# Performance work log

Hardware: AMD Instinct MI355X
Metric: run time of the kernel (lower is better)

The kernel has to match this reference:

```python
import jax, jax.numpy as jnp
import numpy as np

B, T, H, HW = 16, 32, 512, 32  # batch, timesteps, hidden channels, spatial size


def setup_inputs() -> dict:
    key = jax.random.key(0)
    k1, k2, k3, k4, k5 = jax.random.split(key, 5)
    x = jax.random.normal(k1, (B, T, HW, HW), dtype=jnp.float32)
    # cell conv: 1x1, (1 + H) -> 4H, with bias (k=1 default, padding 'same')
    W_conv = jax.random.normal(k2, (4 * H, 1 + H, 1, 1), dtype=jnp.float32) * 0.02
    b_conv = jax.random.normal(k3, (4 * H,), dtype=jnp.float32) * 0.02
    # post conv: 3x3, H -> 1, padding 'same'
    W_post = jax.random.normal(k4, (1, H, 3, 3), dtype=jnp.float32) * 0.02
    b_post = jax.random.normal(k5, (1,), dtype=jnp.float32) * 0.02
    return {"x": x, "W_conv": W_conv, "b_conv": b_conv, "W_post": W_post, "b_post": b_post}


def _post_conv(h, W_post, b_post):
    # NCHW 3x3 'same' conv
    y = jax.lax.conv_general_dilated(
        h, W_post, window_strides=(1, 1), padding="SAME",
        dimension_numbers=("NCHW", "OIHW", "NCHW"))
    return y + b_post[None, :, None, None]


def reference(x, W_conv, b_conv, W_post, b_post):
    Wc = W_conv[:, :, 0, 0]  # [4H, 1+H] -- 1x1 conv is a channel GEMM

    def step(carry, xt):
        h, c = carry  # [B,H,32,32] each; xt [B,1,32,32]
        z = jnp.concatenate([xt, h], axis=1)  # [B,1+H,32,32]
        gates = jnp.einsum("bchw,oc->bohw", z, Wc) + b_conv[None, :, None, None]
        i, f, o, g = jnp.split(gates, 4, axis=1)
        # Faithful to source (non-standard gating):
        c = jax.nn.sigmoid(f) * c + jax.nn.sigmoid(i) + jnp.tanh(g)
        h = jax.nn.sigmoid(o) + jnp.tanh(c)
        y = _post_conv(h, W_post, b_post)  # [B,1,32,32]
        return (h, c), y

    h0 = jnp.zeros((x.shape[0], H, HW, HW), dtype=x.dtype)
    c0 = jnp.zeros_like(h0)
    xs = x[:, :, None, :, :].transpose(1, 0, 2, 3, 4)  # [T,B,1,32,32]
    _, ys = jax.lax.scan(step, (h0, c0), xs)  # ys [T,B,1,32,32]
    out = ys[:, :, 0].transpose(1, 0, 2, 3)  # [B,T,32,32] == cat along dim=1
    return out
```

## Files before the change

### kernel.cpp

```cpp
#include <hip/hip_runtime.h>
#include <cstdint>
#include <cstddef>

#define B_    16
#define T_    32
#define H_    512
#define P_    1024
#define NPOS  16384
#define NG    2048

typedef __attribute__((ext_vector_type(8))) short short8;
typedef __attribute__((ext_vector_type(4))) float f32x4;

__device__ __forceinline__ unsigned short f2bf(float f) {
  uint32_t u = __float_as_uint(f);
  u += 0x7fffu + ((u >> 16) & 1u);
  return (unsigned short)(u >> 16);
}
__device__ __forceinline__ float bflo(uint32_t u) { return __uint_as_float(u << 16); }
__device__ __forceinline__ float bfhi(uint32_t u) { return __uint_as_float(u & 0xffff0000u); }

__device__ __forceinline__ float sigf(float x) {
  return __builtin_amdgcn_rcpf(1.0f + __expf(-x));
}
__device__ __forceinline__ float tanhf_(float x) {
  return 1.0f - 2.0f * __builtin_amdgcn_rcpf(__expf(2.0f * x) + 1.0f);
}

__device__ __forceinline__ void gload_lds16(const void* g, void* l) {
  __builtin_amdgcn_global_load_lds(
      (const __attribute__((address_space(1))) void*)g,
      (__attribute__((address_space(3))) void*)l, 16, 0, 0);
}

__global__ void repack_w(const float* __restrict__ Wc, const float* __restrict__ bconv,
                         unsigned short* __restrict__ Wp, float* __restrict__ w0x,
                         float* __restrict__ bx) {
  int idx = blockIdx.x * 256 + threadIdx.x;
  int r = idx >> 9, k = idx & 511;
  int ch = r >> 2, g = r & 3;
  int o = g * 512 + ch;
  Wp[idx] = f2bf(Wc[o * 513 + 1 + k]);
  if (k == 0) { w0x[r] = Wc[o * 513]; bx[r] = bconv[o]; }
}

__global__ void repack_wpost(const float* __restrict__ Wpost, unsigned short* __restrict__ wppb) {
  int idx = blockIdx.x * 256 + threadIdx.x;
  if (idx >= 16 * 512) return;
  int j = idx >> 9, c = idx & 511;
  float v = (j < 9) ? Wpost[c * 9 + j] : 0.f;
  unsigned short hi = f2bf(v);
  float lo = v - bflo((uint32_t)hi);
  wppb[idx] = hi;
  wppb[16 * 512 + idx] = f2bf(lo);
}

__global__ __launch_bounds__(256, 2)
void lstm_step(const unsigned short* __restrict__ Wp,
               const unsigned short* __restrict__ hprev,
               unsigned short* __restrict__ hnext,
               _Float16* __restrict__ Cst,
               const float* __restrict__ w0x, const float* __restrict__ bxv,
               const float* __restrict__ xin,
               const unsigned short* __restrict__ wppb,
               float* __restrict__ up, int t) {
  __shared__ unsigned short As[256 * 64];
  __shared__ unsigned short Bs[128 * 64];

  const int tid = threadIdx.x;
  const int lane = tid & 63;
  const int wv = tid >> 6;
  const int wm = wv >> 1, wn = wv & 1;
  const int q = lane >> 4, l = lane & 15;

  const int lid = blockIdx.x;
  const int xcd = lid & 7;
  const int s   = lid >> 3;
  const int ny  = xcd * 16 + (s & 15);
  const int rx  = s >> 4;
  const int r0  = rx * 256;
  const int n0  = ny * 128;
  const int ch0 = rx * 64;

  const int srow = tid >> 3;
  const int lchunk = (tid & 7) ^ (srow & 7);
  const unsigned short* gA = Wp    + (size_t)(r0 + srow) * 512 + lchunk * 8;
  const unsigned short* gB = hprev + (size_t)(n0 + srow) * 512 + lchunk * 8;
  char* lA = (char*)As + wv * 1024;
  char* lB = (char*)Bs + wv * 1024;

  f32x4 acc[8][4] = {};

  for (int kc = 0; kc < 512; kc += 64) {
#pragma unroll
    for (int j = 0; j < 8; ++j)
      gload_lds16(gA + (size_t)j * (32 * 512) + kc, lA + j * 4096);
#pragma unroll
    for (int j = 0; j < 4; ++j)
      gload_lds16(gB + (size_t)j * (32 * 512) + kc, lB + j * 4096);
    __syncthreads();

#pragma unroll
    for (int kk = 0; kk < 2; ++kk) {
      short8 af[8], bf_[4];
#pragma unroll
      for (int mi = 0; mi < 8; ++mi) {
        int row = wm * 128 + mi * 16 + l;
        int sidx = row * 64 + (((kk * 4 + q) ^ (row & 7)) * 8);
        af[mi] = *(const short8*)(As + sidx);
      }
#pragma unroll
      for (int ni = 0; ni < 4; ++ni) {
        int row = wn * 64 + ni * 16 + l;
        int sidx = row * 64 + (((kk * 4 + q) ^ (row & 7)) * 8);
        bf_[ni] = *(const short8*)(Bs + sidx);
      }
#pragma unroll
      for (int mi = 0; mi < 8; ++mi)
#pragma unroll
        for (int ni = 0; ni < 4; ++ni)
          acc[mi][ni] = __builtin_amdgcn_mfma_f32_16x16x32_bf16(af[mi], bf_[ni], acc[mi][ni], 0, 0, 0);
    }
    __syncthreads();
  }

  float xv[4]; int posL[4]; size_t cbase[4];
#pragma unroll
  for (int ni = 0; ni < 4; ++ni) {
    posL[ni] = wn * 64 + ni * 16 + l;
    int pos = n0 + posL[ni];
    int b = pos >> 10, p = pos & 1023;
    xv[ni] = xin[((b * T_ + t) << 10) + p];
    cbase[ni] = ((size_t)b << 19) + p;
  }
#pragma unroll
  for (int mi = 0; mi < 8; ++mi) {
    int chl = wm * 32 + mi * 4 + q;
    int rg = r0 + wm * 128 + mi * 16 + q * 4;
    float4 w0 = *(const float4*)(w0x + rg);
    float4 bb = *(const float4*)(bxv + rg);
    int ch = ch0 + chl;
#pragma unroll
    for (int ni = 0; ni < 4; ++ni) {
      f32x4 g = acc[mi][ni];
      float gi = g[0] + w0.x * xv[ni] + bb.x;
      float gf = g[1] + w0.y * xv[ni] + bb.y;
      float go = g[2] + w0.z * xv[ni] + bb.z;
      float gg = g[3] + w0.w * xv[ni] + bb.w;
      size_t cidx = cbase[ni] + ((size_t)ch << 10);
      float cold = (float)Cst[cidx];
      float cn = sigf(gf) * cold + sigf(gi) + tanhf_(gg);
      float hn = sigf(go) + tanhf_(cn);
      Cst[cidx] = (_Float16)cn;
      As[posL[ni] * 64 + (chl ^ ((posL[ni] & 7) << 3))] = f2bf(hn);
    }
  }
  __syncthreads();

  {
    int pl = tid >> 1;
    int cb2 = (tid & 1) << 2;
    const unsigned short* srcrow = As + pl * 64;
    unsigned short* dst = hnext + (size_t)(n0 + pl) * 512 + ch0 + (cb2 << 3);
#pragma unroll
    for (int i = 0; i < 4; ++i)
      ((uint4*)dst)[i] = *(const uint4*)(srcrow + (((cb2 + i) ^ (pl & 7)) << 3));
  }

  {
    const unsigned short* wb_hi = wppb;
    const unsigned short* wb_lo = wppb + 16 * 512;
    const int posg = wv * 32;
    f32x4 a2[2] = {};
#pragma unroll
    for (int kk = 0; kk < 2; ++kk) {
      const int wo = l * 512 + ch0 + kk * 32 + q * 8;
      short8 whi = *(const short8*)(wb_hi + wo);
      short8 wlo = *(const short8*)(wb_lo + wo);
#pragma unroll
      for (int ni2 = 0; ni2 < 2; ++ni2) {
        int row = posg + ni2 * 16 + l;
        int sidx = row * 64 + (((kk * 4 + q) ^ (row & 7)) * 8);
        short8 hf = *(const short8*)(As + sidx);
        a2[ni2] = __builtin_amdgcn_mfma_f32_16x16x32_bf16(whi, hf, a2[ni2], 0, 0, 0);
        a2[ni2] = __builtin_amdgcn_mfma_f32_16x16x32_bf16(wlo, hf, a2[ni2], 0, 0, 0);
      }
    }
#pragma unroll
    for (int ni2 = 0; ni2 < 2; ++ni2) {
      int pix = n0 + posg + ni2 * 16 + l;
#pragma unroll
      for (int r = 0; r < 4; ++r) {
        int j = q * 4 + r;
        if (j < 9)
          up[(size_t)(rx * 9 + j) * NPOS + pix] = a2[ni2][r];
      }
    }
  }
}

__global__ __launch_bounds__(256)
void conv_st2(const float* __restrict__ up, const float* __restrict__ bpost,
              float* __restrict__ out, int t) {
  int idx = blockIdx.x * 256 + threadIdx.x;
  int b = idx >> 10, p = idx & 1023;
  int py = p >> 5, px = p & 31;
  float acc = bpost[0];
#pragma unroll
  for (int dy = -1; dy <= 1; ++dy) {
    int ny = py + dy;
    if ((unsigned)ny > 31u) continue;
#pragma unroll
    for (int dx = -1; dx <= 1; ++dx) {
      int nx = px + dx;
      if ((unsigned)nx > 31u) continue;
      int j = (dy + 1) * 3 + (dx + 1);
      int np = (b << 10) + (ny << 5) + nx;
#pragma unroll
      for (int rx = 0; rx < 8; ++rx)
        acc += up[(size_t)(rx * 9 + j) * NPOS + np];
    }
  }
  out[((b * T_ + t) << 10) + p] = acc;
}

extern "C" void kernel_launch(void* const* d_in, const int* in_sizes, int n_in,
                              void* d_out, int out_size, void* d_ws, size_t ws_size,
                              hipStream_t stream) {
  const float* x     = (const float*)d_in[0];
  const float* Wconv = (const float*)d_in[1];
  const float* bconv = (const float*)d_in[2];
  const float* Wpost = (const float*)d_in[3];
  const float* bpost = (const float*)d_in[4];
  float* out = (float*)d_out;
  char* ws = (char*)d_ws;

  unsigned short* h0   = (unsigned short*)(ws);
  unsigned short* h1   = (unsigned short*)(ws + 16777216);
  _Float16*       Cst  = (_Float16*)(ws + 33554432);
  unsigned short* Wp   = (unsigned short*)(ws + 50331648);
  float*          w0x  = (float*)(ws + 52428800);
  float*          bx   = (float*)(ws + 52436992);
  unsigned short* wppb = (unsigned short*)(ws + 52445184);
  float*          up   = (float*)(ws + 52477952);

  hipMemsetAsync(h0, 0, 16777216, stream);
  hipMemsetAsync(Cst, 0, 16777216, stream);
  repack_w<<<4096, 256, 0, stream>>>(Wconv, bconv, Wp, w0x, bx);
  repack_wpost<<<32, 256, 0, stream>>>(Wpost, wppb);

  unsigned short* hp = h0;
  unsigned short* hn = h1;
  for (int t = 0; t < T_; ++t) {
    lstm_step<<<1024, 256, 0, stream>>>(Wp, hp, hn, Cst, w0x, bx, x, wppb, up, t);
    conv_st2<<<64, 256, 0, stream>>>(up, bpost, out, t);
    unsigned short* tmp = hp; hp = hn; hn = tmp;
  }
}
```

Before: 1.763 ms.

## Fold previous step's post-conv reduction into next LSTM step with double-buffered partials

The separate conv_st2 launch after every timestep is removed. Instead, the first 16 threads of each lstm_step block reduce the previous step's 3x3 post-conv partial sums for 16 pixels and write out[t-1], with the partial buffer now double-buffered across steps; a single conv_st2 launch handles the final step. The GEMM's first K-chunk global->LDS loads are issued before this extra work, and each later chunk load is moved to the end of the previous iteration. The intent is to cut 31 small kernel launches and their serialization gaps. The cost is extra scattered reads in a few threads of each GEMM block and one more workspace buffer.

```diff
diff --git a/kernel.cpp b/kernel.cpp
--- a/kernel.cpp
+++ b/kernel.cpp
@@ -63,7 +63,8 @@
                const float* __restrict__ w0x, const float* __restrict__ bxv,
                const float* __restrict__ xin,
                const unsigned short* __restrict__ wppb,
-               float* __restrict__ up, int t) {
+               const float* __restrict__ upPrev, float* __restrict__ upCur,
+               const float* __restrict__ bpost, float* __restrict__ out, int t) {
   __shared__ unsigned short As[256 * 64];
   __shared__ unsigned short Bs[128 * 64];
 
@@ -91,13 +92,37 @@
 
   f32x4 acc[8][4] = {};
 
+#pragma unroll
+  for (int j = 0; j < 8; ++j)
+    gload_lds16(gA + (size_t)j * (32 * 512), lA + j * 4096);
+#pragma unroll
+  for (int j = 0; j < 4; ++j)
+    gload_lds16(gB + (size_t)j * (32 * 512), lB + j * 4096);
+
+  if (t > 0 && tid < 16) {
+    int pix = lid * 16 + tid;
+    int b = pix >> 10, p = pix & 1023;
+    int py = p >> 5, px = p & 31;
+    float a = bpost[0];
+#pragma unroll
+    for (int dy = -1; dy <= 1; ++dy) {
+      int nyy = py + dy;
+      if ((unsigned)nyy > 31u) continue;
+#pragma unroll
+      for (int dx = -1; dx <= 1; ++dx) {
+        int nx = px + dx;
+        if ((unsigned)nx > 31u) continue;
+        int j = (dy + 1) * 3 + (dx + 1);
+        int np = (b << 10) + (nyy << 5) + nx;
+#pragma unroll
+        for (int rr = 0; rr < 8; ++rr)
+          a += upPrev[(size_t)(rr * 9 + j) * NPOS + np];
+      }
+    }
+    out[((b * T_ + (t - 1)) << 10) + p] = a;
+  }
+
   for (int kc = 0; kc < 512; kc += 64) {
-#pragma unroll
-    for (int j = 0; j < 8; ++j)
-      gload_lds16(gA + (size_t)j * (32 * 512) + kc, lA + j * 4096);
-#pragma unroll
-    for (int j = 0; j < 4; ++j)
-      gload_lds16(gB + (size_t)j * (32 * 512) + kc, lB + j * 4096);
     __syncthreads();
 
 #pragma unroll
@@ -122,6 +147,16 @@
           acc[mi][ni] = __builtin_amdgcn_mfma_f32_16x16x32_bf16(af[mi], bf_[ni], acc[mi][ni], 0, 0, 0);
     }
     __syncthreads();
+
+    if (kc < 448) {
+      int kn = kc + 64;
+#pragma unroll
+      for (int j = 0; j < 8; ++j)
+        gload_lds16(gA + (size_t)j * (32 * 512) + kn, lA + j * 4096);
+#pragma unroll
+      for (int j = 0; j < 4; ++j)
+        gload_lds16(gB + (size_t)j * (32 * 512) + kn, lB + j * 4096);
+    }
   }
 
   float xv[4]; int posL[4]; size_t cbase[4];
@@ -193,7 +228,7 @@
       for (int r = 0; r < 4; ++r) {
         int j = q * 4 + r;
         if (j < 9)
-          up[(size_t)(rx * 9 + j) * NPOS + pix] = a2[ni2][r];
+          upCur[(size_t)(rx * 9 + j) * NPOS + pix] = a2[ni2][r];
       }
     }
   }
@@ -217,8 +252,8 @@
       int j = (dy + 1) * 3 + (dx + 1);
       int np = (b << 10) + (ny << 5) + nx;
 #pragma unroll
-      for (int rx = 0; rx < 8; ++rx)
-        acc += up[(size_t)(rx * 9 + j) * NPOS + np];
+      for (int rxx = 0; rxx < 8; ++rxx)
+        acc += up[(size_t)(rxx * 9 + j) * NPOS + np];
     }
   }
   out[((b * T_ + t) << 10) + p] = acc;
@@ -242,7 +277,8 @@
   float*          w0x  = (float*)(ws + 52428800);
   float*          bx   = (float*)(ws + 52436992);
   unsigned short* wppb = (unsigned short*)(ws + 52445184);
-  float*          up   = (float*)(ws + 52477952);
+  float*          up0  = (float*)(ws + 52477952);
+  float*          up1  = (float*)(ws + 57196544);
 
   hipMemsetAsync(h0, 0, 16777216, stream);
   hipMemsetAsync(Cst, 0, 16777216, stream);
@@ -252,8 +288,11 @@
   unsigned short* hp = h0;
   unsigned short* hn = h1;
   for (int t = 0; t < T_; ++t) {
-    lstm_step<<<1024, 256, 0, stream>>>(Wp, hp, hn, Cst, w0x, bx, x, wppb, up, t);
-    conv_st2<<<64, 256, 0, stream>>>(up, bpost, out, t);
+    const float* upPrev = (t & 1) ? up0 : up1;
+    float*       upCur  = (t & 1) ? up1 : up0;
+    lstm_step<<<1024, 256, 0, stream>>>(Wp, hp, hn, Cst, w0x, bx, x, wppb,
+                                        upPrev, upCur, bpost, out, t);
     unsigned short* tmp = hp; hp = hn; hn = tmp;
   }
-}
+  conv_st2<<<64, 256, 0, stream>>>((T_ & 1) ? up0 : up1, bpost, out, T_ - 1);
+}
```

Result: slower. 1.841 ms (+4.4%).
